# Performance work log

Hardware: AMD Instinct MI355X
Metric: run time of the kernel (lower is better)

The kernel has to match this reference:

```python
import jax, jax.numpy as jnp
import numpy as np

N = 200000
E = 3200000
IN_C = 256
HID = 16
OUT_C = 16
EPS = 1e-5


def gcn_conv(x, W, b, src, dst):
    # PyG GCNConv: linear first, then normalized scatter-add with self-loops
    h = x @ W  # [N, F_out]
    loop = jnp.arange(N)
    src2 = jnp.concatenate([src, loop])
    dst2 = jnp.concatenate([dst, loop])
    deg = jax.ops.segment_sum(jnp.ones_like(dst2, dtype=h.dtype), dst2, num_segments=N)
    dinv = jnp.where(deg > 0, jax.lax.rsqrt(deg), 0.0)
    norm = dinv[src2] * dinv[dst2]  # [E+N]
    msg = h[src2] * norm[:, None]
    out = jax.ops.segment_sum(msg, dst2, num_segments=N)
    return out + b


def batch_norm(x, gamma, beta):
    mu = jnp.mean(x, axis=0)
    var = jnp.var(x, axis=0)
    return gamma * (x - mu) * jax.lax.rsqrt(var + EPS) + beta


def setup_inputs() -> dict:
    key = jax.random.key(0)
    ks = jax.random.split(key, 8)
    x = jax.random.normal(ks[0], (N, IN_C), dtype=jnp.float32)
    edge_index = jax.random.randint(ks[1], (2, E), 0, N, dtype=jnp.int64)
    W1 = jax.random.normal(ks[2], (IN_C, HID), dtype=jnp.float32) / np.sqrt(IN_C)
    b1 = jnp.zeros((HID,), jnp.float32)
    g1 = jnp.ones((HID,), jnp.float32)
    be1 = jnp.zeros((HID,), jnp.float32)
    W2 = jax.random.normal(ks[3], (HID, HID), dtype=jnp.float32) / np.sqrt(HID)
    b2 = jnp.zeros((HID,), jnp.float32)
    g2 = jnp.ones((HID,), jnp.float32)
    be2 = jnp.zeros((HID,), jnp.float32)
    W3 = jax.random.normal(ks[4], (HID, OUT_C), dtype=jnp.float32) / np.sqrt(HID)
    b3 = jnp.zeros((OUT_C,), jnp.float32)
    return {"x": x, "edge_index": edge_index, "W1": W1, "b1": b1, "g1": g1,
            "be1": be1, "W2": W2, "b2": b2, "g2": g2, "be2": be2,
            "W3": W3, "b3": b3}


def reference(x, edge_index, W1, b1, g1, be1, W2, b2, g2, be2, W3, b3):
    src, dst = edge_index[0], edge_index[1]
    h = jax.nn.relu(batch_norm(gcn_conv(x, W1, b1, src, dst), g1, be1))
    h = jax.nn.relu(batch_norm(gcn_conv(h, W2, b2, src, dst), g2, be2))
    return gcn_conv(h, W3, b3, src, dst)
```

## Files before the change

### kernel.cpp

```cpp
#include <hip/hip_runtime.h>
#include <hip/hip_bf16.h>
#include <stdint.h>

#define EPSV 1e-5f
#define BKLG 10
#define BK 1024
#define P1CHUNK 16384


__global__ void k_zero(int* __restrict__ bcnt, float* __restrict__ stats) {
  int t = threadIdx.x;
  bcnt[t] = 0;
  if (t < 64) stats[t] = 0.f;
}


__global__ __launch_bounds__(256) void k_bcount(const int* __restrict__ e32, int E, int NB,
                                                int* __restrict__ bcnt) {
  __shared__ int cnt[256];
  int t = threadIdx.x;
  cnt[t] = 0;
  __syncthreads();
  int e0 = blockIdx.x * P1CHUNK;
  int e1 = min(e0 + P1CHUNK, E);
  for (int i = e0 + t; i < e1; i += 256) {
    int d = e32[(size_t)E + i];
    atomicAdd(&cnt[d >> BKLG], 1);
  }
  __syncthreads();
  if (t < NB) {
    int c = cnt[t];
    if (c) atomicAdd(&bcnt[t], c);
  }
}

__global__ void k_bscan(const int* __restrict__ bcnt, int NB, int E, int N,
                        int* __restrict__ ticket, int* __restrict__ bbeg,
                        int* __restrict__ offs) {
  __shared__ int sd[256];
  int t = threadIdx.x;
  int v = (t < NB) ? bcnt[t] : 0;
  sd[t] = v;
  __syncthreads();
  for (int st = 1; st < 256; st <<= 1) {
    int add = (t >= st) ? sd[t - st] : 0;
    __syncthreads();
    sd[t] += add;
    __syncthreads();
  }
  int ex = sd[t] - v;
  if (t < NB) {
    ticket[t] = ex;
    bbeg[t] = ex;
  }
  if (t == 0) {
    bbeg[NB] = E;
    offs[N] = E;
  }
}

__global__ __launch_bounds__(256) void k_bin(const int* __restrict__ e32, int E, int NB,
                                             int* __restrict__ ticket,
                                             unsigned* __restrict__ staged) {
  __shared__ int cnt[256];
  __shared__ int base[256];
  int t = threadIdx.x;
  int e0 = blockIdx.x * P1CHUNK;
  int e1 = min(e0 + P1CHUNK, E);
  if (t < NB) cnt[t] = 0;
  __syncthreads();
  for (int i = e0 + t; i < e1; i += 256) {
    int d = e32[(size_t)E + i];
    atomicAdd(&cnt[d >> BKLG], 1);
  }
  __syncthreads();
  if (t < NB) {
    int c = cnt[t];
    base[t] = c ? atomicAdd(&ticket[t], c) : 0;
    cnt[t] = 0;
  }
  __syncthreads();
  for (int i = e0 + t; i < e1; i += 256) {
    int s = e32[i];
    int d = e32[(size_t)E + i];
    int b = d >> BKLG;
    int l = atomicAdd(&cnt[b], 1);
    staged[base[b] + l] = (unsigned)s | ((unsigned)(d & (BK - 1)) << 18);
  }
}

__global__ __launch_bounds__(256) void k_place(const unsigned* __restrict__ staged,
                                               const int* __restrict__ bbeg, int N,
                                               int* __restrict__ csr,
                                               int* __restrict__ offs,
                                               float* __restrict__ dinv) {
  __shared__ int hist[BK];
  __shared__ int lpos[BK];
  __shared__ int sd[256];
  int b = blockIdx.x;
  int n0 = b << BKLG;
  int t = threadIdx.x;
  for (int i = t; i < BK; i += 256) hist[i] = 0;
  __syncthreads();
  int beg = bbeg[b], endp = bbeg[b + 1];
  for (int j = beg + t; j < endp; j += 256) {
    unsigned v = staged[j];
    atomicAdd(&hist[v >> 18], 1);
  }
  __syncthreads();
  int i0 = t * 4;
  int h0 = hist[i0], h1 = hist[i0 + 1], h2 = hist[i0 + 2], h3 = hist[i0 + 3];
  int s = h0 + h1 + h2 + h3;
  sd[t] = s;
  __syncthreads();
  for (int st = 1; st < 256; st <<= 1) {
    int add = (t >= st) ? sd[t - st] : 0;
    __syncthreads();
    sd[t] += add;
    __syncthreads();
  }
  int ex = sd[t] - s;
  int l0 = ex, l1 = ex + h0, l2 = l1 + h1, l3 = l2 + h2;
  lpos[i0] = beg + l0;
  lpos[i0 + 1] = beg + l1;
  lpos[i0 + 2] = beg + l2;
  lpos[i0 + 3] = beg + l3;
  int node = n0 + i0;
  if (node < N) {
    offs[node] = beg + l0;
    dinv[node] = rsqrtf((float)(h0 + 1));
  }
  if (node + 1 < N) {
    offs[node + 1] = beg + l1;
    dinv[node + 1] = rsqrtf((float)(h1 + 1));
  }
  if (node + 2 < N) {
    offs[node + 2] = beg + l2;
    dinv[node + 2] = rsqrtf((float)(h2 + 1));
  }
  if (node + 3 < N) {
    offs[node + 3] = beg + l3;
    dinv[node + 3] = rsqrtf((float)(h3 + 1));
  }
  __syncthreads();
  for (int j = beg + t; j < endp; j += 256) {
    unsigned v = staged[j];
    int dl = (int)(v >> 18);
    int p = atomicAdd(&lpos[dl], 1);
    csr[p] = (int)(v & 0x3FFFFu);
  }
}


__global__ __launch_bounds__(256) void k_gemm1(const float* __restrict__ x,
                                               const float* __restrict__ W,
                                               const float* __restrict__ dinv, int N,
                                               float* __restrict__ hs) {
  int row = blockIdx.x * 256 + threadIdx.x;
  if (row >= N) return;
  const float4* xr = (const float4*)(x + (size_t)row * 256);
  float acc[16];
#pragma unroll
  for (int c = 0; c < 16; c++) acc[c] = 0.f;
#pragma unroll 8
  for (int j = 0; j < 64; j++) {
    float4 v = xr[j];
    const float* w0 = W + j * 64;
#pragma unroll
    for (int c = 0; c < 16; c++) {
      float t0 = fmaf(v.x, w0[c], acc[c]);
      float t1 = fmaf(v.y, w0[16 + c], t0);
      float t2 = fmaf(v.z, w0[32 + c], t1);
      acc[c] = fmaf(v.w, w0[48 + c], t2);
    }
  }
  float dv = dinv[row];
  float4* o4 = (float4*)(hs + (size_t)row * 16);
#pragma unroll
  for (int i = 0; i < 4; i++)
    o4[i] = make_float4(acc[i * 4] * dv, acc[i * 4 + 1] * dv, acc[i * 4 + 2] * dv,
                        acc[i * 4 + 3] * dv);
}

__global__ void k_agg(const float* __restrict__ hs, const int* __restrict__ csr,
                      const int* __restrict__ offs, const float* __restrict__ dinv,
                      const float* __restrict__ bias, int N, float* __restrict__ out) {
  int g = blockIdx.x * 256 + threadIdx.x;
  int node = g >> 2, q = g & 3;
  if (node >= N) return;
  int beg = offs[node], end = offs[node + 1];
  const float4* hs4 = (const float4*)hs;
  float4 a = hs4[(size_t)node * 4 + q];
  for (int j = beg; j < end; j++) {
    int s = csr[j];
    float4 v = hs4[(size_t)s * 4 + q];
    a.x += v.x; a.y += v.y; a.z += v.z; a.w += v.w;
  }
  float dv = dinv[node];
  float4 b = ((const float4*)bias)[q];
  ((float4*)out)[(size_t)node * 4 + q] =
      make_float4(fmaf(a.x, dv, b.x), fmaf(a.y, dv, b.y), fmaf(a.z, dv, b.z), fmaf(a.w, dv, b.w));
}

__global__ void k_bnstats(const float* __restrict__ o, int N, float* __restrict__ stats) {
  __shared__ float ss[256];
  __shared__ float sq[256];
  int t = threadIdx.x;
  int c = t & 15;
  int r = blockIdx.x * 16 + (t >> 4);
  int stride = gridDim.x * 16;
  float s = 0.f, q = 0.f;
  for (; r < N; r += stride) {
    float v = o[(size_t)r * 16 + c];
    s += v;
    q = fmaf(v, v, q);
  }
  ss[t] = s;
  sq[t] = q;
  __syncthreads();
  for (int st = 128; st >= 16; st >>= 1) {
    if (t < st) { ss[t] += ss[t + st]; sq[t] += sq[t + st]; }
    __syncthreads();
  }
  if (t < 16) {
    atomicAdd(&stats[t], ss[t]);
    atomicAdd(&stats[16 + t], sq[t]);
  }
}

__global__ void k_affine(const float* __restrict__ stats, const float* __restrict__ g,
                         const float* __restrict__ be, float invN, float* __restrict__ a,
                         float* __restrict__ s) {
  int c = threadIdx.x;
  if (c < 16) {
    float mean = stats[c] * invN;
    float var = stats[16 + c] * invN - mean * mean;
    float av = g[c] * rsqrtf(var + EPSV);
    a[c] = av;
    s[c] = be[c] - mean * av;
  }
}

__global__ void k_gemm_small(const float* __restrict__ in, const float* __restrict__ a,
                             const float* __restrict__ s, const float* __restrict__ W,
                             const float* __restrict__ dinv, int N, float* __restrict__ out) {
  int row = blockIdx.x * 256 + threadIdx.x;
  if (row >= N) return;
  const float4* in4 = (const float4*)(in + (size_t)row * 16);
  float v[16];
#pragma unroll
  for (int i = 0; i < 4; i++) {
    float4 tv = in4[i];
    v[i * 4 + 0] = tv.x; v[i * 4 + 1] = tv.y; v[i * 4 + 2] = tv.z; v[i * 4 + 3] = tv.w;
  }
#pragma unroll
  for (int c = 0; c < 16; c++) v[c] = fmaxf(fmaf(a[c], v[c], s[c]), 0.f);
  float acc[16];
#pragma unroll
  for (int c = 0; c < 16; c++) acc[c] = 0.f;
#pragma unroll
  for (int k = 0; k < 16; k++) {
#pragma unroll
    for (int c = 0; c < 16; c++) acc[c] = fmaf(v[k], W[k * 16 + c], acc[c]);
  }
  float dv = dinv[row];
  float4* o4 = (float4*)(out + (size_t)row * 16);
#pragma unroll
  for (int i = 0; i < 4; i++)
    o4[i] = make_float4(acc[i * 4] * dv, acc[i * 4 + 1] * dv, acc[i * 4 + 2] * dv,
                        acc[i * 4 + 3] * dv);
}


extern "C" void kernel_launch(void* const* d_in, const int* in_sizes, int n_in,
                              void* d_out, int out_size, void* d_ws, size_t ws_size,
                              hipStream_t stream) {
  const float* x = (const float*)d_in[0];
  const int* eidx = (const int*)d_in[1];
  const float* W1 = (const float*)d_in[2];
  const float* b1 = (const float*)d_in[3];
  const float* g1 = (const float*)d_in[4];
  const float* be1 = (const float*)d_in[5];
  const float* W2 = (const float*)d_in[6];
  const float* b2 = (const float*)d_in[7];
  const float* g2 = (const float*)d_in[8];
  const float* be2 = (const float*)d_in[9];
  const float* W3 = (const float*)d_in[10];
  const float* b3 = (const float*)d_in[11];
  float* out = (float*)d_out;

  int N = in_sizes[0] / 256;
  int E = in_sizes[1] / 2;
  int NB = (N + BK - 1) / BK;

  char* w = (char*)d_ws;
  float* hs = (float*)w;
  int* csr = (int*)(w + (size_t)N * 16 * 4);
  char* p = w + (size_t)N * 16 * 4 + (size_t)E * 4;
  int* offs = (int*)p;
  p += (size_t)(N + 4) * 4;
  float* dinv = (float*)p;
  p += (size_t)N * 4;
  float* stats1 = (float*)p;
  float* stats2 = stats1 + 32;
  float* a1 = stats2 + 32;
  float* s1 = a1 + 16;
  float* a2 = s1 + 16;
  float* s2 = a2 + 16;
  int* bcnt = (int*)(s2 + 16);
  int* bbeg = bcnt + 256;
  int* ticket = bbeg + 260;

  unsigned* staged = (unsigned*)hs;

  int gN = (N + 255) / 256;
  int gQ = (N * 4 + 255) / 256;
  int gB = (E + P1CHUNK - 1) / P1CHUNK;

  k_zero<<<1, 256, 0, stream>>>(bcnt, stats1);
  k_bcount<<<gB, 256, 0, stream>>>(eidx, E, NB, bcnt);
  k_bscan<<<1, 256, 0, stream>>>(bcnt, NB, E, N, ticket, bbeg, offs);
  k_bin<<<gB, 256, 0, stream>>>(eidx, E, NB, ticket, staged);
  k_place<<<NB, 256, 0, stream>>>(staged, bbeg, N, csr, offs, dinv);

  float* o = out;
  float invN = 1.f / (float)N;

  k_gemm1<<<gN, 256, 0, stream>>>(x, W1, dinv, N, hs);
  k_agg<<<gQ, 256, 0, stream>>>(hs, csr, offs, dinv, b1, N, o);
  k_bnstats<<<256, 256, 0, stream>>>(o, N, stats1);
  k_affine<<<1, 64, 0, stream>>>(stats1, g1, be1, invN, a1, s1);
  k_gemm_small<<<gN, 256, 0, stream>>>(o, a1, s1, W2, dinv, N, hs);
  k_agg<<<gQ, 256, 0, stream>>>(hs, csr, offs, dinv, b2, N, o);
  k_bnstats<<<256, 256, 0, stream>>>(o, N, stats2);
  k_affine<<<1, 64, 0, stream>>>(stats2, g2, be2, invN, a2, s2);
  k_gemm_small<<<gN, 256, 0, stream>>>(o, a2, s2, W3, dinv, N, hs);
  k_agg<<<gQ, 256, 0, stream>>>(hs, csr, offs, dinv, b3, N, out);
}
```

Baseline: 694.1 us.

## Replace CSR build and gather with bucketed LDS atomic aggregation

Drops the per-node CSR placement pass and aggregates edges directly from the destination-bucketed staging array. Each 1024-thread block owns a bucket of 1024 nodes and accumulates neighbor features into a skewed 64KB shared-memory tile with LDS float atomics. BatchNorm statistics are fused into the aggregation epilogue, which removes the separate stats kernels. The cost is 16 LDS atomics per edge, only NB (~196) large blocks so occupancy is low, and a floating-point summation order that is no longer deterministic.

```diff
diff --git a/kernel.cpp b/kernel.cpp
--- a/kernel.cpp
+++ b/kernel.cpp
@@ -34,9 +34,8 @@
   }
 }
 
-__global__ void k_bscan(const int* __restrict__ bcnt, int NB, int E, int N,
-                        int* __restrict__ ticket, int* __restrict__ bbeg,
-                        int* __restrict__ offs) {
+__global__ void k_bscan(const int* __restrict__ bcnt, int NB, int E,
+                        int* __restrict__ ticket, int* __restrict__ bbeg) {
   __shared__ int sd[256];
   int t = threadIdx.x;
   int v = (t < NB) ? bcnt[t] : 0;
@@ -53,10 +52,7 @@
     ticket[t] = ex;
     bbeg[t] = ex;
   }
-  if (t == 0) {
-    bbeg[NB] = E;
-    offs[N] = E;
-  }
+  if (t == 0) bbeg[NB] = E;
 }
 
 __global__ __launch_bounds__(256) void k_bin(const int* __restrict__ e32, int E, int NB,
@@ -89,65 +85,20 @@
   }
 }
 
-__global__ __launch_bounds__(256) void k_place(const unsigned* __restrict__ staged,
+__global__ __launch_bounds__(256) void k_dinv2(const unsigned* __restrict__ staged,
                                                const int* __restrict__ bbeg, int N,
-                                               int* __restrict__ csr,
-                                               int* __restrict__ offs,
                                                float* __restrict__ dinv) {
   __shared__ int hist[BK];
-  __shared__ int lpos[BK];
-  __shared__ int sd[256];
-  int b = blockIdx.x;
+  int b = blockIdx.x, t = threadIdx.x;
+  for (int i = t; i < BK; i += 256) hist[i] = 0;
+  __syncthreads();
+  int beg = bbeg[b], endp = bbeg[b + 1];
+  for (int j = beg + t; j < endp; j += 256) atomicAdd(&hist[staged[j] >> 18], 1);
+  __syncthreads();
   int n0 = b << BKLG;
-  int t = threadIdx.x;
-  for (int i = t; i < BK; i += 256) hist[i] = 0;
-  __syncthreads();
-  int beg = bbeg[b], endp = bbeg[b + 1];
-  for (int j = beg + t; j < endp; j += 256) {
-    unsigned v = staged[j];
-    atomicAdd(&hist[v >> 18], 1);
-  }
-  __syncthreads();
-  int i0 = t * 4;
-  int h0 = hist[i0], h1 = hist[i0 + 1], h2 = hist[i0 + 2], h3 = hist[i0 + 3];
-  int s = h0 + h1 + h2 + h3;
-  sd[t] = s;
-  __syncthreads();
-  for (int st = 1; st < 256; st <<= 1) {
-    int add = (t >= st) ? sd[t - st] : 0;
-    __syncthreads();
-    sd[t] += add;
-    __syncthreads();
-  }
-  int ex = sd[t] - s;
-  int l0 = ex, l1 = ex + h0, l2 = l1 + h1, l3 = l2 + h2;
-  lpos[i0] = beg + l0;
-  lpos[i0 + 1] = beg + l1;
-  lpos[i0 + 2] = beg + l2;
-  lpos[i0 + 3] = beg + l3;
-  int node = n0 + i0;
-  if (node < N) {
-    offs[node] = beg + l0;
-    dinv[node] = rsqrtf((float)(h0 + 1));
-  }
-  if (node + 1 < N) {
-    offs[node + 1] = beg + l1;
-    dinv[node + 1] = rsqrtf((float)(h1 + 1));
-  }
-  if (node + 2 < N) {
-    offs[node + 2] = beg + l2;
-    dinv[node + 2] = rsqrtf((float)(h2 + 1));
-  }
-  if (node + 3 < N) {
-    offs[node + 3] = beg + l3;
-    dinv[node + 3] = rsqrtf((float)(h3 + 1));
-  }
-  __syncthreads();
-  for (int j = beg + t; j < endp; j += 256) {
-    unsigned v = staged[j];
-    int dl = (int)(v >> 18);
-    int p = atomicAdd(&lpos[dl], 1);
-    csr[p] = (int)(v & 0x3FFFFu);
+  for (int i = t; i < BK; i += 256) {
+    int gn = n0 + i;
+    if (gn < N) dinv[gn] = rsqrtf((float)(hist[i] + 1));
   }
 }
 
@@ -182,49 +133,69 @@
                         acc[i * 4 + 3] * dv);
 }
 
-__global__ void k_agg(const float* __restrict__ hs, const int* __restrict__ csr,
-                      const int* __restrict__ offs, const float* __restrict__ dinv,
-                      const float* __restrict__ bias, int N, float* __restrict__ out) {
-  int g = blockIdx.x * 256 + threadIdx.x;
-  int node = g >> 2, q = g & 3;
-  if (node >= N) return;
-  int beg = offs[node], end = offs[node + 1];
-  const float4* hs4 = (const float4*)hs;
-  float4 a = hs4[(size_t)node * 4 + q];
-  for (int j = beg; j < end; j++) {
-    int s = csr[j];
-    float4 v = hs4[(size_t)s * 4 + q];
-    a.x += v.x; a.y += v.y; a.z += v.z; a.w += v.w;
-  }
-  float dv = dinv[node];
-  float4 b = ((const float4*)bias)[q];
-  ((float4*)out)[(size_t)node * 4 + q] =
-      make_float4(fmaf(a.x, dv, b.x), fmaf(a.y, dv, b.y), fmaf(a.z, dv, b.z), fmaf(a.w, dv, b.w));
-}
-
-__global__ void k_bnstats(const float* __restrict__ o, int N, float* __restrict__ stats) {
-  __shared__ float ss[256];
-  __shared__ float sq[256];
-  int t = threadIdx.x;
+__global__ __launch_bounds__(1024) void k_agg_lds(const float* __restrict__ hs,
+                                                  const unsigned* __restrict__ staged,
+                                                  const int* __restrict__ bbeg,
+                                                  const float* __restrict__ dinv,
+                                                  const float* __restrict__ bias, int N,
+                                                  float* __restrict__ out,
+                                                  float* __restrict__ stats, int do_stats) {
+  __shared__ float acc[BK * 16];
+  int b = blockIdx.x, t = threadIdx.x;
+  int n0 = b << BKLG;
+#pragma unroll
+  for (int k = 0; k < 16; k++) {
+    int i = t + k * 1024;
+    int node = i >> 4, c = i & 15;
+    int gn = n0 + node;
+    float v = (gn < N) ? hs[(size_t)gn * 16 + c] : 0.f;
+    acc[(node << 4) + ((c + node) & 15)] = v;
+  }
+  __syncthreads();
+  int beg = bbeg[b], endp = bbeg[b + 1];
+  for (int j = beg + t; j < endp; j += 1024) {
+    unsigned v = staged[j];
+    int s = (int)(v & 0x3FFFFu);
+    int dl = (int)(v >> 18);
+    const float4* r4 = (const float4*)(hs + (size_t)s * 16);
+    float4 q0 = r4[0], q1 = r4[1], q2 = r4[2], q3 = r4[3];
+    float rv[16];
+    rv[0] = q0.x; rv[1] = q0.y; rv[2] = q0.z; rv[3] = q0.w;
+    rv[4] = q1.x; rv[5] = q1.y; rv[6] = q1.z; rv[7] = q1.w;
+    rv[8] = q2.x; rv[9] = q2.y; rv[10] = q2.z; rv[11] = q2.w;
+    rv[12] = q3.x; rv[13] = q3.y; rv[14] = q3.z; rv[15] = q3.w;
+    int basei = dl << 4;
+#pragma unroll
+    for (int k = 0; k < 16; k++) atomicAdd(&acc[basei + ((k + dl) & 15)], rv[k]);
+  }
+  __syncthreads();
+  float s_sum = 0.f, s_sq = 0.f;
   int c = t & 15;
-  int r = blockIdx.x * 16 + (t >> 4);
-  int stride = gridDim.x * 16;
-  float s = 0.f, q = 0.f;
-  for (; r < N; r += stride) {
-    float v = o[(size_t)r * 16 + c];
-    s += v;
-    q = fmaf(v, v, q);
-  }
-  ss[t] = s;
-  sq[t] = q;
-  __syncthreads();
-  for (int st = 128; st >= 16; st >>= 1) {
-    if (t < st) { ss[t] += ss[t + st]; sq[t] += sq[t + st]; }
+  float bi = bias[c];
+#pragma unroll
+  for (int k = 0; k < 16; k++) {
+    int i = t + k * 1024;
+    int node = i >> 4;
+    int gn = n0 + node;
+    if (gn < N) {
+      float val = acc[(node << 4) + ((c + node) & 15)];
+      float o = fmaf(val, dinv[gn], bi);
+      out[(size_t)gn * 16 + c] = o;
+      s_sum += o;
+      s_sq = fmaf(o, o, s_sq);
+    }
+  }
+  if (do_stats) {
     __syncthreads();
-  }
-  if (t < 16) {
-    atomicAdd(&stats[t], ss[t]);
-    atomicAdd(&stats[16 + t], sq[t]);
+    acc[t] = s_sum;
+    acc[1024 + t] = s_sq;
+    __syncthreads();
+    for (int st = 512; st >= 16; st >>= 1) {
+      if (t < st) { acc[t] += acc[t + st]; acc[1024 + t] += acc[1024 + t + st]; }
+      __syncthreads();
+    }
+    if (t < 16) atomicAdd(&stats[t], acc[t]);
+    else if (t < 32) atomicAdd(&stats[16 + (t - 16)], acc[1024 + (t - 16)]);
   }
 }
 
@@ -295,10 +266,8 @@
 
   char* w = (char*)d_ws;
   float* hs = (float*)w;
-  int* csr = (int*)(w + (size_t)N * 16 * 4);
+  unsigned* staged = (unsigned*)(w + (size_t)N * 16 * 4);
   char* p = w + (size_t)N * 16 * 4 + (size_t)E * 4;
-  int* offs = (int*)p;
-  p += (size_t)(N + 4) * 4;
   float* dinv = (float*)p;
   p += (size_t)N * 4;
   float* stats1 = (float*)p;
@@ -311,29 +280,24 @@
   int* bbeg = bcnt + 256;
   int* ticket = bbeg + 260;
 
-  unsigned* staged = (unsigned*)hs;
-
   int gN = (N + 255) / 256;
-  int gQ = (N * 4 + 255) / 256;
   int gB = (E + P1CHUNK - 1) / P1CHUNK;
 
   k_zero<<<1, 256, 0, stream>>>(bcnt, stats1);
   k_bcount<<<gB, 256, 0, stream>>>(eidx, E, NB, bcnt);
-  k_bscan<<<1, 256, 0, stream>>>(bcnt, NB, E, N, ticket, bbeg, offs);
+  k_bscan<<<1, 256, 0, stream>>>(bcnt, NB, E, ticket, bbeg);
   k_bin<<<gB, 256, 0, stream>>>(eidx, E, NB, ticket, staged);
-  k_place<<<NB, 256, 0, stream>>>(staged, bbeg, N, csr, offs, dinv);
+  k_dinv2<<<NB, 256, 0, stream>>>(staged, bbeg, N, dinv);
 
   float* o = out;
   float invN = 1.f / (float)N;
 
   k_gemm1<<<gN, 256, 0, stream>>>(x, W1, dinv, N, hs);
-  k_agg<<<gQ, 256, 0, stream>>>(hs, csr, offs, dinv, b1, N, o);
-  k_bnstats<<<256, 256, 0, stream>>>(o, N, stats1);
+  k_agg_lds<<<NB, 1024, 0, stream>>>(hs, staged, bbeg, dinv, b1, N, o, stats1, 1);
   k_affine<<<1, 64, 0, stream>>>(stats1, g1, be1, invN, a1, s1);
   k_gemm_small<<<gN, 256, 0, stream>>>(o, a1, s1, W2, dinv, N, hs);
-  k_agg<<<gQ, 256, 0, stream>>>(hs, csr, offs, dinv, b2, N, o);
-  k_bnstats<<<256, 256, 0, stream>>>(o, N, stats2);
+  k_agg_lds<<<NB, 1024, 0, stream>>>(hs, staged, bbeg, dinv, b2, N, o, stats2, 1);
   k_affine<<<1, 64, 0, stream>>>(stats2, g2, be2, invN, a2, s2);
   k_gemm_small<<<gN, 256, 0, stream>>>(o, a2, s2, W3, dinv, N, hs);
-  k_agg<<<gQ, 256, 0, stream>>>(hs, csr, offs, dinv, b3, N, out);
-}
+  k_agg_lds<<<NB, 1024, 0, stream>>>(hs, staged, bbeg, dinv, b3, N, out, nullptr, 0);
+}
```

After: 1.502 ms. +116.4%, slower.
